# Kernel tuning notes

Measured on AMD Instinct MI355X. Metric: run time of the kernel, lower is better.

## Reference

```python
import jax, jax.numpy as jnp
import numpy as np

B, E, K, S, D, H, C = 8192, 8, 2, 32, 3072, 256, 100  # batch, experts, fix_points, img size, flat dim, hidden, classes


def setup_inputs() -> dict:
    key = jax.random.key(0)
    ks = jax.random.split(key, 6)
    return {
        "x": jax.random.normal(ks[0], (B, 3, S, S), jnp.float32),
        "coeffs_t": jax.random.uniform(ks[1], (K,), jnp.float32),
        "router_w": jax.random.normal(ks[2], (K, D, E), jnp.float32) * 0.02,
        "router_b": jnp.zeros((K, E), jnp.float32),
        "w1": jax.random.normal(ks[3], (E, K, D, H), jnp.float32) * 0.02,
        "b1": jnp.zeros((E, K, H), jnp.float32),
        "w2": jax.random.normal(ks[4], (E, K, H, C), jnp.float32) * 0.02,
        "b2": jnp.zeros((E, K, C), jnp.float32),
    }


def reference(x, coeffs_t, router_w, router_b, w1, b1, w2, b2):
    xf = x.reshape(x.shape[0], -1)  # [B, D]
    # Curve parameter blend: W = sum_k coeffs_t[k] * W_k (CurveParameter semantics)
    Wr = jnp.einsum('k,kde->de', coeffs_t, router_w)
    br = jnp.einsum('k,ke->e', coeffs_t, router_b)
    # Router: top-1 expert index per sample
    idx = jnp.argmax(xf @ Wr + br, axis=-1)  # [B] int
    # Blended expert weights
    W1 = jnp.einsum('k,ekdh->edh', coeffs_t, w1)
    B1 = jnp.einsum('k,ekh->eh', coeffs_t, b1)
    W2 = jnp.einsum('k,ekhc->ehc', coeffs_t, w2)
    B2 = jnp.einsum('k,ekc->ec', coeffs_t, b2)
    # Expert MLP (computed for all experts with static shapes, then top-1 gather;
    # identical math to torch's boolean-mask dispatch/scatter)
    h = jax.nn.gelu(jnp.einsum('bd,edh->beh', xf, W1) + B1, approximate=False)  # [B,E,H]
    o = jnp.einsum('beh,ehc->bec', h, W2) + B2  # [B,E,C]
    return jnp.take_along_axis(o, idx[:, None, None], axis=1)[:, 0, :]  # [B,C]
```

## Files before the change

### kernel.cpp

```cpp
#include <hip/hip_runtime.h>
#include <math.h>

#define B_  8192
#define E_  8
#define D_  3072
#define H_  256
#define C_  100
#define DH_ (D_*H_)
#define HC_ (H_*C_)
#define KS_ 4
#define KSEG_ (D_/KS_)
#define RKS_ 16
#define RSEG_ (D_/RKS_)
#define RB_ (B_/256)
#define NTMAX_ 136
#define NT2MAX_ 528
#define NCH_ (D_/32)
#define CHW_ 10240

#define MEGA_R_   (RB_*RKS_)
#define MEGA_W1_  (E_*NCH_)
#define MEGA_W2_  (C_*E_)
#define MEGA_BB_  3
#define MEGA_TOT_ (MEGA_R_ + MEGA_W1_ + MEGA_W2_ + MEGA_BB_)

typedef __attribute__((ext_vector_type(4))) float  f32x4;
typedef __attribute__((ext_vector_type(8))) __bf16 bf16x8;
typedef __attribute__((ext_vector_type(8))) unsigned short ush8;
typedef __attribute__((ext_vector_type(4))) unsigned short ush4;

#define GLOAD_LDS16(g, l) __builtin_amdgcn_global_load_lds( \
    (const __attribute__((address_space(1))) void*)(g),     \
    (__attribute__((address_space(3))) void*)(l), 16, 0, 0)

__device__ inline unsigned short bf16_rne(float f) {
    unsigned u = __builtin_bit_cast(unsigned, f);
    unsigned r = (u + 0x7FFFu + ((u >> 16) & 1u)) >> 16;
    return (unsigned short)r;
}
__device__ inline float bf16_f(unsigned short h) {
    unsigned u = ((unsigned)h) << 16;
    return __builtin_bit_cast(float, u);
}

#define MISC_B1_ (E_*H_/4)
#define MISC_B2_ (E_*C_/4)

__global__ __launch_bounds__(256) void mega_k(
        const float* __restrict__ x, const float* __restrict__ rw,
        const float* __restrict__ w1, const float* __restrict__ w2,
        const float* __restrict__ b1, const float* __restrict__ b2,
        unsigned short* __restrict__ Whi, unsigned short* __restrict__ Wlo,
        unsigned short* __restrict__ W2thi, unsigned short* __restrict__ W2tlo,
        float* __restrict__ B1b, float* __restrict__ B2b,
        double* __restrict__ lpart, const float* __restrict__ coeffs) {
    __shared__ char smem[36864];
    int bid = blockIdx.x;
    int t = threadIdx.x;

    if (bid < MEGA_R_) {
        float  (*xs)[64][33] = (float(*)[64][33])smem;
        double (*wls)[8]     = (double(*)[8])(smem + 33792);
        int w = t >> 6, lane = t & 63;
        int rowblk = (bid & (RB_ - 1)) * 256;
        int s2     = bid >> 5;
        int kbase  = s2 * RSEG_;
        int row0   = rowblk + w * 64;
        double c0 = (double)coeffs[0], c1 = (double)coeffs[1];

        double acc[8] = {0, 0, 0, 0, 0, 0, 0, 0};

        for (int kb = 0; kb < RSEG_; kb += 32) {
            #pragma unroll
            for (int it = 0; it < 8; it++) {
                int i = lane + it * 64;
                int r = i >> 3, c4 = i & 7;
                *(float4*)&xs[w][r][c4 * 4] =
                    *(const float4*)(x + (size_t)(row0 + r) * D_ + kbase + kb + c4 * 4);
            }
            if (w == 0) {
                #pragma unroll
                for (int it = 0; it < 4; it++) {
                    int i = lane + it * 64;
                    int k = i >> 3, ee = i & 7;
                    wls[k][ee] = c0 * (double)rw[(size_t)(kbase + kb + k) * 8 + ee]
                               + c1 * (double)rw[(size_t)(D_ + kbase + kb + k) * 8 + ee];
                }
            }
            __syncthreads();
            #pragma unroll
            for (int kk = 0; kk < 32; kk++) {
                double xv = (double)xs[w][lane][kk];
                double2 w01 = *(const double2*)&wls[kk][0];
                double2 w23 = *(const double2*)&wls[kk][2];
                double2 w45 = *(const double2*)&wls[kk][4];
                double2 w67 = *(const double2*)&wls[kk][6];
                acc[0] = fma(xv, w01.x, acc[0]);
                acc[1] = fma(xv, w01.y, acc[1]);
                acc[2] = fma(xv, w23.x, acc[2]);
                acc[3] = fma(xv, w23.y, acc[3]);
                acc[4] = fma(xv, w45.x, acc[4]);
                acc[5] = fma(xv, w45.y, acc[5]);
                acc[6] = fma(xv, w67.x, acc[6]);
                acc[7] = fma(xv, w67.y, acc[7]);
            }
            __syncthreads();
        }
        size_t base = ((size_t)s2 * B_ + row0 + lane) * 8;
        #pragma unroll
        for (int ee = 0; ee < 8; ee++) lpart[base + ee] = acc[ee];

    } else if (bid < MEGA_R_ + MEGA_W1_) {
        int lid = bid - MEGA_R_;
        int e  = lid / NCH_;
        int ci = lid - e * NCH_;
        int d0 = ci * 32;
        unsigned short* thi = (unsigned short*)smem;
        unsigned short* tlo = thi + 32 * 256;
        float c0 = coeffs[0], c1 = coeffs[1];
        const float* pa = w1 + ((size_t)(e * 2 + 0) * D_ + d0) * H_;
        const float* pb = w1 + ((size_t)(e * 2 + 1) * D_ + d0) * H_;
        #pragma unroll
        for (int it = 0; it < 8; it++) {
            int i4 = t + it * 256;
            float4 va = *(const float4*)(pa + (size_t)i4 * 4);
            float4 vb = *(const float4*)(pb + (size_t)i4 * 4);
            float vv[4] = {c0 * va.x + c1 * vb.x, c0 * va.y + c1 * vb.y,
                           c0 * va.z + c1 * vb.z, c0 * va.w + c1 * vb.w};
            unsigned short h4[4], l4[4];
            #pragma unroll
            for (int j = 0; j < 4; j++) {
                unsigned short hi = bf16_rne(vv[j]);
                h4[j] = hi;
                l4[j] = bf16_rne(vv[j] - bf16_f(hi));
            }
            *(ush4*)&thi[i4 * 4] = *(const ush4*)h4;
            *(ush4*)&tlo[i4 * 4] = *(const ush4*)l4;
        }
        __syncthreads();
        #pragma unroll
        for (int it = 0; it < 4; it++) {
            int j = t + it * 256;
            int h = j >> 2, d8 = (j & 3) * 8;
            unsigned short vh[8], vl[8];
            #pragma unroll
            for (int k2 = 0; k2 < 8; k2++) {
                vh[k2] = thi[(d8 + k2) * 256 + h];
                vl[k2] = tlo[(d8 + k2) * 256 + h];
            }
            size_t g = ((size_t)e * NCH_ + ci) * CHW_ + (size_t)h * 40 + d8;
            *(ush8*)(Whi + g) = *(const ush8*)vh;
            *(ush8*)(Wlo + g) = *(const ush8*)vl;
        }

    } else if (bid < MEGA_R_ + MEGA_W1_ + MEGA_W2_) {
        int lid = bid - (MEGA_R_ + MEGA_W1_);
        int c = lid % C_, e = lid / C_;
        int k = t;
        float c0 = coeffs[0], c1 = coeffs[1];
        float v = c0 * w2[((size_t)(e * 2 + 0) * H_ + k) * C_ + c]
                + c1 * w2[((size_t)(e * 2 + 1) * H_ + k) * C_ + c];
        unsigned short hi = bf16_rne(v);
        W2thi[(size_t)(e * C_ + c) * H_ + k] = hi;
        W2tlo[(size_t)(e * C_ + c) * H_ + k] = bf16_rne(v - bf16_f(hi));

    } else {
        int gid = (bid - (MEGA_R_ + MEGA_W1_ + MEGA_W2_)) * 256 + t;
        float c0 = coeffs[0], c1 = coeffs[1];
        if (gid < MISC_B1_) {
            const float4* p = (const float4*)b1;
            int e = gid / (H_ / 4), r = gid - e * (H_ / 4);
            float4 a = p[(e * 2 + 0) * (H_ / 4) + r];
            float4 bq = p[(e * 2 + 1) * (H_ / 4) + r];
            float4 o;
            o.x = c0 * a.x + c1 * bq.x;
            o.y = c0 * a.y + c1 * bq.y;
            o.z = c0 * a.z + c1 * bq.z;
            o.w = c0 * a.w + c1 * bq.w;
            ((float4*)B1b)[gid] = o;
        } else if (gid < MISC_B1_ + MISC_B2_) {
            int g2 = gid - MISC_B1_;
            const float4* p = (const float4*)b2;
            int e = g2 / (C_ / 4), r = g2 - e * (C_ / 4);
            float4 a = p[(e * 2 + 0) * (C_ / 4) + r];
            float4 bq = p[(e * 2 + 1) * (C_ / 4) + r];
            float4 o;
            o.x = c0 * a.x + c1 * bq.x;
            o.y = c0 * a.y + c1 * bq.y;
            o.z = c0 * a.z + c1 * bq.z;
            o.w = c0 * a.w + c1 * bq.w;
            ((float4*)B2b)[g2] = o;
        }
    }
}

__global__ __launch_bounds__(256) void argmax_hist_k(
        const double* __restrict__ lpart, const float* __restrict__ rb,
        const float* __restrict__ coeffs, int* __restrict__ idx,
        int* __restrict__ hist) {
    __shared__ int scnt[8];
    int t = threadIdx.x;
    if (t < 8) scnt[t] = 0;
    __syncthreads();
    int b = blockIdx.x * 256 + t;
    double c0 = (double)coeffs[0], c1 = (double)coeffs[1];
    double l[8];
    #pragma unroll
    for (int e = 0; e < 8; e++)
        l[e] = c0 * (double)rb[e] + c1 * (double)rb[8 + e];
    for (int s2 = 0; s2 < RKS_; s2++) {
        const double2* pp = (const double2*)(lpart + ((size_t)s2 * B_ + b) * 8);
        double2 v0 = pp[0], v1 = pp[1], v2 = pp[2], v3 = pp[3];
        l[0] += v0.x; l[1] += v0.y; l[2] += v1.x; l[3] += v1.y;
        l[4] += v2.x; l[5] += v2.y; l[6] += v3.x; l[7] += v3.y;
    }
    double best = -1e300;
    int bi = 0;
    #pragma unroll
    for (int e = 0; e < 8; e++)
        if (l[e] > best) { best = l[e]; bi = e; }
    idx[b] = bi;
    atomicAdd(&scnt[bi], 1);
    __syncthreads();
    if (t < 8) hist[blockIdx.x * 8 + t] = scnt[t];
}

__global__ __launch_bounds__(256) void scatter2_k(
        const int* __restrict__ idx, const int* __restrict__ hist,
        int* __restrict__ order, int* __restrict__ cnt, int* __restrict__ off,
        int* __restrict__ tmap, int* __restrict__ tmap2, int* __restrict__ ntl) {
    __shared__ int sbi[256];
    __shared__ int stot[8];
    __shared__ int sbase[8];
    int b0 = blockIdx.x, t = threadIdx.x;
    int b = b0 * 256 + t;
    int mybi = idx[b];
    sbi[t] = mybi;
    if (t < 8) {
        int tot = 0, pre = 0;
        for (int bb = 0; bb < RB_; bb++) {
            int h = hist[bb * 8 + t];
            if (bb < b0) pre += h;
            tot += h;
        }
        stot[t] = tot;
        sbase[t] = pre;
    }
    __syncthreads();
    if (t < 8) {
        int o = 0;
        for (int j = 0; j < t; j++) o += stot[j];
        sbase[t] += o;
    }
    __syncthreads();
    int rank = 0;
    for (int i = 0; i < 256; i++) {
        int v = sbi[i];
        rank += (i < t && v == mybi) ? 1 : 0;
    }
    order[sbase[mybi] + rank] = (mybi << 16) | b;

    if (b0 == 0 && t == 0) {
        int s = 0;
        for (int e = 0; e < E_; e++) { cnt[e] = stot[e]; off[e] = s; s += stot[e]; }
        int nt = 0;
        for (int e = 0; e < E_; e++)
            for (int t0 = 0; t0 < stot[e]; t0 += 64)
                tmap[nt++] = (e << 16) | t0;
        ntl[0] = nt;
        int nt2 = 0;
        for (int e = 0; e < E_; e++)
            for (int t0 = 0; t0 < stot[e]; t0 += 16)
                tmap2[nt2++] = (e << 16) | t0;
        ntl[1] = nt2;
    }
}

template<int MODE>
__global__ __launch_bounds__(256, 3) void gemm1_t(
        const float* __restrict__ x, const unsigned short* __restrict__ Whi,
        const unsigned short* __restrict__ Wlo, const int* __restrict__ order,
        const int* __restrict__ cnt, const int* __restrict__ off,
        const int* __restrict__ tmap, const int* __restrict__ ntl,
        float* __restrict__ dst) {
    int tid = blockIdx.y;
    if (tid >= ntl[0]) return;
    int tm = tmap[tid];
    int e = tm >> 16, tile0 = tm & 0xFFFF;
    int ce = cnt[e];
    int s = blockIdx.x;

    __shared__ int rows[64];
    __shared__ unsigned short xs_hi[64 * 40];
    __shared__ unsigned short xs_lo[64 * 40];
    __shared__ unsigned short ws_hi[256 * 40];
    __shared__ unsigned short ws_lo[256 * 40];

    int t = threadIdx.x;
    if (t < 64) {
        int i = tile0 + t;
        rows[t] = (i < ce) ? (order[off[e] + i] & 0xFFFF) : -1;
    }
    __syncthreads();
    int xrow0 = rows[0];

    int lane = t & 63, w = t >> 6;
    int lr = lane & 15, quad = lane >> 4;
    int kbase = s * KSEG_;
    int wuni = t & ~63;

    f32x4 acc[4][4];
    #pragma unroll
    for (int mt = 0; mt < 4; mt++)
        #pragma unroll
        for (int nt = 0; nt < 4; nt++)
            acc[mt][nt] = (f32x4){0.f, 0.f, 0.f, 0.f};

    for (int kb = 0; kb < KSEG_; kb += 32) {
        {
            int ci = (kbase + kb) >> 5;
            const unsigned short* ph = Whi + ((size_t)e * NCH_ + ci) * CHW_;
            const unsigned short* pl = Wlo + ((size_t)e * NCH_ + ci) * CHW_;
            #pragma unroll
            for (int j = 0; j < 5; j++) {
                GLOAD_LDS16(ph + ((size_t)(j * 256 + t)) * 8,
                            ws_hi + (size_t)(j * 256 + wuni) * 8);
                GLOAD_LDS16(pl + ((size_t)(j * 256 + t)) * 8,
                            ws_lo + (size_t)(j * 256 + wuni) * 8);
            }
        }
        #pragma unroll
        for (int it = 0; it < 2; it++) {
            int i = t + it * 256;
            int rr = i >> 3, sg = i & 7;
            int row = rows[rr];
            if (row < 0) row = xrow0;
            float4 v = *(const float4*)(x + (size_t)row * D_ + kbase + kb + sg * 4);
            unsigned short h4[4], l4[4];
            float vv[4] = {v.x, v.y, v.z, v.w};
            #pragma unroll
            for (int j = 0; j < 4; j++) {
                unsigned short hi = bf16_rne(vv[j]);
                h4[j] = hi;
                l4[j] = bf16_rne(vv[j] - bf16_f(hi));
            }
            *(ush4*)&xs_hi[rr * 40 + sg * 4] = *(const ush4*)h4;
            *(ush4*)&xs_lo[rr * 40 + sg * 4] = *(const ush4*)l4;
        }
        __syncthreads();

        bf16x8 ah[4], al[4], bh[4], bl[4];
        #pragma unroll
        for (int mt = 0; mt < 4; mt++) {
            ah[mt] = __builtin_bit_cast(bf16x8, *(const ush8*)&xs_hi[(mt * 16 + lr) * 40 + quad * 8]);
            al[mt] = __builtin_bit_cast(bf16x8, *(const ush8*)&xs_lo[(mt * 16 + lr) * 40 + quad * 8]);
        }
        #pragma unroll
        for (int nt = 0; nt < 4; nt++) {
            int col = w * 64 + nt * 16 + lr;
            bh[nt] = __builtin_bit_cast(bf16x8, *(const ush8*)&ws_hi[col * 40 + quad * 8]);
            bl[nt] = __builtin_bit_cast(bf16x8, *(const ush8*)&ws_lo[col * 40 + quad * 8]);
        }
        #pragma unroll
        for (int mt = 0; mt < 4; mt++)
            #pragma unroll
            for (int nt = 0; nt < 4; nt++) {
                acc[mt][nt] = __builtin_amdgcn_mfma_f32_16x16x32_bf16(ah[mt], bh[nt], acc[mt][nt], 0, 0, 0);
                acc[mt][nt] = __builtin_amdgcn_mfma_f32_16x16x32_bf16(al[mt], bh[nt], acc[mt][nt], 0, 0, 0);
                acc[mt][nt] = __builtin_amdgcn_mfma_f32_16x16x32_bf16(ah[mt], bl[nt], acc[mt][nt], 0, 0, 0);
                acc[mt][nt] = __builtin_amdgcn_mfma_f32_16x16x32_bf16(al[mt], bl[nt], acc[mt][nt], 0, 0, 0);
            }
        __syncthreads();
    }

    size_t p0 = (size_t)off[e] + tile0;
    if (MODE == 1) {
        float* dp = dst + ((size_t)s * B_ + p0) * H_;
        #pragma unroll
        for (int mt = 0; mt < 4; mt++) {
            int rl = mt * 16 + quad * 4;
            #pragma unroll
            for (int nt = 0; nt < 4; nt++) {
                int col = w * 64 + nt * 16 + lr;
                #pragma unroll
                for (int rg = 0; rg < 4; rg++) {
                    if (tile0 + rl + rg < ce)
                        dp[(size_t)(rl + rg) * H_ + col] = acc[mt][nt][rg];
                }
            }
        }
    } else {
        #pragma unroll
        for (int mt = 0; mt < 4; mt++) {
            int rl = mt * 16 + quad * 4;
            #pragma unroll
            for (int nt = 0; nt < 4; nt++) {
                int col = w * 64 + nt * 16 + lr;
                #pragma unroll
                for (int rg = 0; rg < 4; rg++) {
                    if (tile0 + rl + rg < ce)
                        atomicAdd(&dst[(p0 + rl + rg) * H_ + col], acc[mt][nt][rg]);
                }
            }
        }
    }
}

__global__ __launch_bounds__(256) void bias_gelu_k(
        float* __restrict__ hws, const float* __restrict__ B1b,
        const int* __restrict__ order) {
    int gid = blockIdx.x * 256 + threadIdx.x;
    int p = gid >> 6, c4 = (gid & 63) * 4;
    int e = order[p] >> 16;
    float4 v = *(const float4*)(hws + (size_t)p * H_ + c4);
    const float4 bb = *(const float4*)(B1b + e * H_ + c4);
    float pre[4] = {v.x + bb.x, v.y + bb.y, v.z + bb.z, v.w + bb.w};
    float4 o;
    o.x = 0.5f * pre[0] * (1.0f + erff(pre[0] * 0.70710678118654752440f));
    o.y = 0.5f * pre[1] * (1.0f + erff(pre[1] * 0.70710678118654752440f));
    o.z = 0.5f * pre[2] * (1.0f + erff(pre[2] * 0.70710678118654752440f));
    o.w = 0.5f * pre[3] * (1.0f + erff(pre[3] * 0.70710678118654752440f));
    *(float4*)(hws + (size_t)p * H_ + c4) = o;
}

template<int FUSE>
__global__ __launch_bounds__(256) void gemm2_t(
        const float* __restrict__ hsrc,
        const unsigned short* __restrict__ W2thi, const unsigned short* __restrict__ W2tlo,
        const float* __restrict__ B1b, const float* __restrict__ B2b,
        const int* __restrict__ order, const int* __restrict__ cnt,
        const int* __restrict__ off, const int* __restrict__ tmap2,
        const int* __restrict__ ntl, float* __restrict__ out) {
    int tid = blockIdx.x;
    if (tid >= ntl[1]) return;
    int tm = tmap2[tid];
    int e = tm >> 16, tile0 = tm & 0xFFFF;
    int ce = cnt[e];

    __shared__ int rows[16];
    __shared__ float red[3][64][28];

    int t = threadIdx.x;
    if (t < 16) {
        int i = tile0 + t;
        rows[t] = (i < ce) ? (order[off[e] + i] & 0xFFFF) : -1;
    }
    __syncthreads();

    int lane = t & 63, w = t >> 6;
    int m = lane & 15, q = lane >> 4;
    int p = off[e] + tile0 + ((tile0 + m < ce) ? m : 0);

    f32x4 acc[7];
    #pragma unroll
    for (int nt = 0; nt < 7; nt++) acc[nt] = (f32x4){0.f, 0.f, 0.f, 0.f};

    const unsigned short* w2h = W2thi + (size_t)e * C_ * H_;
    const unsigned short* w2l = W2tlo + (size_t)e * C_ * H_;

    #pragma unroll
    for (int si = 0; si < 2; si++) {
        int s = w * 2 + si;
        int k0 = s * 32 + q * 8;
        size_t o = (size_t)p * H_ + k0;
        float f[8];
        if (FUSE) {
            float4 a0 = *(const float4*)(hsrc + o);
            float4 a1 = *(const float4*)(hsrc + o + 4);
            #pragma unroll
            for (int s2 = 1; s2 < KS_; s2++) {
                const float* sp = hsrc + (size_t)s2 * B_ * H_ + o;
                float4 b0 = *(const float4*)sp;
                float4 b1v = *(const float4*)(sp + 4);
                a0.x += b0.x; a0.y += b0.y; a0.z += b0.z; a0.w += b0.w;
                a1.x += b1v.x; a1.y += b1v.y; a1.z += b1v.z; a1.w += b1v.w;
            }
            float4 bb0 = *(const float4*)(B1b + e * H_ + k0);
            float4 bb1 = *(const float4*)(B1b + e * H_ + k0 + 4);
            float pre[8] = {a0.x + bb0.x, a0.y + bb0.y, a0.z + bb0.z, a0.w + bb0.w,
                            a1.x + bb1.x, a1.y + bb1.y, a1.z + bb1.z, a1.w + bb1.w};
            #pragma unroll
            for (int j = 0; j < 8; j++)
                f[j] = 0.5f * pre[j] * (1.0f + erff(pre[j] * 0.70710678118654752440f));
        } else {
            float4 v0 = *(const float4*)(hsrc + o);
            float4 v1 = *(const float4*)(hsrc + o + 4);
            f[0] = v0.x; f[1] = v0.y; f[2] = v0.z; f[3] = v0.w;
            f[4] = v1.x; f[5] = v1.y; f[6] = v1.z; f[7] = v1.w;
        }
        unsigned short hh[8], lo[8];
        #pragma unroll
        for (int j = 0; j < 8; j++) {
            unsigned short hi = bf16_rne(f[j]);
            hh[j] = hi;
            lo[j] = bf16_rne(f[j] - bf16_f(hi));
        }
        bf16x8 ah = __builtin_bit_cast(bf16x8, *(const ush8*)hh);
        bf16x8 al = __builtin_bit_cast(bf16x8, *(const ush8*)lo);
        #pragma unroll
        for (int nt = 0; nt < 7; nt++) {
            size_t bo = (size_t)(nt * 16 + m) * H_ + k0;
            bf16x8 bh = __builtin_bit_cast(bf16x8, *(const ush8*)(w2h + bo));
            bf16x8 bl = __builtin_bit_cast(bf16x8, *(const ush8*)(w2l + bo));
            acc[nt] = __builtin_amdgcn_mfma_f32_16x16x32_bf16(ah, bh, acc[nt], 0, 0, 0);
            acc[nt] = __builtin_amdgcn_mfma_f32_16x16x32_bf16(al, bh, acc[nt], 0, 0, 0);
            acc[nt] = __builtin_amdgcn_mfma_f32_16x16x32_bf16(ah, bl, acc[nt], 0, 0, 0);
            acc[nt] = __builtin_amdgcn_mfma_f32_16x16x32_bf16(al, bl, acc[nt], 0, 0, 0);
        }
    }

    if (w > 0) {
        #pragma unroll
        for (int nt = 0; nt < 7; nt++)
            #pragma unroll
            for (int i = 0; i < 4; i++)
                red[w - 1][lane][nt * 4 + i] = acc[nt][i];
    }
    __syncthreads();
    if (w == 0) {
        #pragma unroll
        for (int nt = 0; nt < 7; nt++)
            #pragma unroll
            for (int i = 0; i < 4; i++)
                acc[nt][i] = ((acc[nt][i] + red[0][lane][nt * 4 + i])
                              + red[1][lane][nt * 4 + i]) + red[2][lane][nt * 4 + i];
        #pragma unroll
        for (int nt = 0; nt < 7; nt++) {
            int c = nt * 16 + m;
            if (c >= C_) continue;
            float bias = B2b[e * C_ + c];
            #pragma unroll
            for (int i = 0; i < 4; i++) {
                int grow = q * 4 + i;
                if (tile0 + grow < ce)
                    out[(size_t)rows[grow] * C_ + c] = acc[nt][i] + bias;
            }
        }
    }
}

extern "C" void kernel_launch(void* const* d_in, const int* in_sizes, int n_in,
                              void* d_out, int out_size, void* d_ws, size_t ws_size,
                              hipStream_t stream) {
    const float* x        = (const float*)d_in[0];
    const float* coeffs   = (const float*)d_in[1];
    const float* router_w = (const float*)d_in[2];
    const float* router_b = (const float*)d_in[3];
    const float* w1       = (const float*)d_in[4];
    const float* b1       = (const float*)d_in[5];
    const float* w2       = (const float*)d_in[6];
    const float* b2       = (const float*)d_in[7];
    float* out = (float*)d_out;

    unsigned short* Whi   = (unsigned short*)d_ws;
    unsigned short* Wlo   = Whi + (size_t)E_ * NCH_ * CHW_;
    unsigned short* W2thi = Wlo + (size_t)E_ * NCH_ * CHW_;
    unsigned short* W2tlo = W2thi + (size_t)E_ * C_ * H_;
    float* B1b  = (float*)(W2tlo + (size_t)E_ * C_ * H_);
    float* B2b  = B1b + (size_t)E_ * H_;
    int* order  = (int*)(B2b + E_ * C_);
    int* cnt    = order + B_;
    int* off    = cnt + E_;
    int* tmap   = off + E_;
    int* tmap2  = tmap + NTMAX_;
    int* ntl    = tmap2 + NT2MAX_;
    int* idx    = ntl + 4;
    int* hist   = idx + B_;
    float* hws  = (float*)(hist + 256);
    double* lpart = (double*)hws;

    size_t prefix_bytes = (size_t)((char*)hws - (char*)d_ws);
    int use_part = (ws_size >= prefix_bytes + (size_t)KS_ * B_ * H_ * sizeof(float) + 256) ? 1 : 0;

    mega_k<<<dim3(MEGA_TOT_), 256, 0, stream>>>(
        x, router_w, w1, w2, b1, b2, Whi, Wlo, W2thi, W2tlo, B1b, B2b,
        lpart, coeffs);

    argmax_hist_k<<<dim3(RB_), 256, 0, stream>>>(lpart, router_b, coeffs, idx, hist);
    scatter2_k<<<dim3(RB_), 256, 0, stream>>>(idx, hist, order, cnt, off,
                                              tmap, tmap2, ntl);

    if (use_part) {
        gemm1_t<1><<<dim3(KS_, NTMAX_), 256, 0, stream>>>(x, Whi, Wlo, order, cnt,
                                                          off, tmap, ntl, hws);
        gemm2_t<1><<<dim3(NT2MAX_), 256, 0, stream>>>(hws, W2thi, W2tlo, B1b, B2b,
                                                      order, cnt, off, tmap2, ntl, out);
    } else {
        hipMemsetAsync(hws, 0, (size_t)B_ * H_ * sizeof(float), stream);
        gemm1_t<0><<<dim3(KS_, NTMAX_), 256, 0, stream>>>(x, Whi, Wlo, order, cnt,
                                                          off, tmap, ntl, hws);
        bias_gelu_k<<<dim3(B_ * H_ / 4 / 256), 256, 0, stream>>>(hws, B1b, order);
        gemm2_t<0><<<dim3(NT2MAX_), 256, 0, stream>>>(hws, W2thi, W2tlo, B1b, B2b,
                                                      order, cnt, off, tmap2, ntl, out);
    }
}
```

Baseline: 323.0 us.

## Double-buffer router loads via async global-to-LDS with swizzle, shrink mega blocks

The router section of the preprocessing kernel now loads x tiles asynchronously into LDS with global_load_lds, double-buffered, and uses an XOR swizzle to avoid bank conflicts. The blended router weights for the next chunk are prefetched into registers and written to the other buffer after compute, which removes one barrier per iteration. Blocks shrink to 128 threads, with twice as many router blocks, and the other sections are adjusted to loop over twice as many elements. This aims to hide global load latency in the fp64 router GEMV, at the cost of more blocks and a more complex indexing scheme.

```diff
diff --git a/kernel.cpp b/kernel.cpp
--- a/kernel.cpp
+++ b/kernel.cpp
@@ -18,10 +18,10 @@
 #define NCH_ (D_/32)
 #define CHW_ 10240
 
-#define MEGA_R_   (RB_*RKS_)
+#define MEGA_R_   ((B_/128)*RKS_)
 #define MEGA_W1_  (E_*NCH_)
 #define MEGA_W2_  (C_*E_)
-#define MEGA_BB_  3
+#define MEGA_BB_  6
 #define MEGA_TOT_ (MEGA_R_ + MEGA_W1_ + MEGA_W2_ + MEGA_BB_)
 
 typedef __attribute__((ext_vector_type(4))) float  f32x4;
@@ -46,7 +46,7 @@
 #define MISC_B1_ (E_*H_/4)
 #define MISC_B2_ (E_*C_/4)
 
-__global__ __launch_bounds__(256) void mega_k(
+__global__ __launch_bounds__(128) void mega_k(
         const float* __restrict__ x, const float* __restrict__ rw,
         const float* __restrict__ w1, const float* __restrict__ w2,
         const float* __restrict__ b1, const float* __restrict__ b2,
@@ -59,42 +59,64 @@
     int t = threadIdx.x;
 
     if (bid < MEGA_R_) {
-        float  (*xs)[64][33] = (float(*)[64][33])smem;
-        double (*wls)[8]     = (double(*)[8])(smem + 33792);
+        float*  xs  = (float*)smem;
+        double* wls = (double*)(smem + 32768);
         int w = t >> 6, lane = t & 63;
-        int rowblk = (bid & (RB_ - 1)) * 256;
-        int s2     = bid >> 5;
+        int rowblk = (bid & 63) * 128;
+        int s2     = bid >> 6;
         int kbase  = s2 * RSEG_;
-        int row0   = rowblk + w * 64;
+        int row0w  = rowblk + w * 64;
         double c0 = (double)coeffs[0], c1 = (double)coeffs[1];
 
+        int c4L = (lane & 7) ^ ((lane >> 3) & 7);
+
         double acc[8] = {0, 0, 0, 0, 0, 0, 0, 0};
 
+        #pragma unroll
+        for (int j = 0; j < 8; j++) {
+            int r = j * 8 + (lane >> 3);
+            GLOAD_LDS16(x + (size_t)(row0w + r) * D_ + kbase + c4L * 4,
+                        smem + (size_t)w * 8192 + j * 1024);
+        }
+        {
+            #pragma unroll
+            for (int it = 0; it < 2; it++) {
+                int i = t + it * 128;
+                int k = i >> 3, ee = i & 7;
+                wls[k * 8 + ee] = c0 * (double)rw[(size_t)(kbase + k) * 8 + ee]
+                                + c1 * (double)rw[(size_t)(D_ + kbase + k) * 8 + ee];
+            }
+        }
+        __syncthreads();
+
+        int p = 0;
         for (int kb = 0; kb < RSEG_; kb += 32) {
-            #pragma unroll
-            for (int it = 0; it < 8; it++) {
-                int i = lane + it * 64;
-                int r = i >> 3, c4 = i & 7;
-                *(float4*)&xs[w][r][c4 * 4] =
-                    *(const float4*)(x + (size_t)(row0 + r) * D_ + kbase + kb + c4 * 4);
-            }
-            if (w == 0) {
+            int nxt = p ^ 1;
+            float rwa0 = 0.f, rwb0 = 0.f, rwa1 = 0.f, rwb1 = 0.f;
+            int more = (kb + 32 < RSEG_);
+            if (more) {
                 #pragma unroll
-                for (int it = 0; it < 4; it++) {
-                    int i = lane + it * 64;
-                    int k = i >> 3, ee = i & 7;
-                    wls[k][ee] = c0 * (double)rw[(size_t)(kbase + kb + k) * 8 + ee]
-                               + c1 * (double)rw[(size_t)(D_ + kbase + kb + k) * 8 + ee];
+                for (int j = 0; j < 8; j++) {
+                    int r = j * 8 + (lane >> 3);
+                    GLOAD_LDS16(x + (size_t)(row0w + r) * D_ + kbase + kb + 32 + c4L * 4,
+                                smem + (size_t)(nxt * 2 + w) * 8192 + j * 1024);
                 }
-            }
-            __syncthreads();
+                int i0 = t, i1 = t + 128;
+                rwa0 = rw[(size_t)(kbase + kb + 32 + (i0 >> 3)) * 8 + (i0 & 7)];
+                rwb0 = rw[(size_t)(D_ + kbase + kb + 32 + (i0 >> 3)) * 8 + (i0 & 7)];
+                rwa1 = rw[(size_t)(kbase + kb + 32 + (i1 >> 3)) * 8 + (i1 & 7)];
+                rwb1 = rw[(size_t)(D_ + kbase + kb + 32 + (i1 >> 3)) * 8 + (i1 & 7)];
+            }
+
+            const float*  xw = xs + (size_t)(p * 2 + w) * 2048 + lane * 32;
+            const double* wp = wls + (size_t)p * 256;
             #pragma unroll
             for (int kk = 0; kk < 32; kk++) {
-                double xv = (double)xs[w][lane][kk];
-                double2 w01 = *(const double2*)&wls[kk][0];
-                double2 w23 = *(const double2*)&wls[kk][2];
-                double2 w45 = *(const double2*)&wls[kk][4];
-                double2 w67 = *(const double2*)&wls[kk][6];
+                double xv = (double)xw[((((kk >> 2) ^ (lane & 7)) << 2) + (kk & 3))];
+                double2 w01 = *(const double2*)&wp[kk * 8 + 0];
+                double2 w23 = *(const double2*)&wp[kk * 8 + 2];
+                double2 w45 = *(const double2*)&wp[kk * 8 + 4];
+                double2 w67 = *(const double2*)&wp[kk * 8 + 6];
                 acc[0] = fma(xv, w01.x, acc[0]);
                 acc[1] = fma(xv, w01.y, acc[1]);
                 acc[2] = fma(xv, w23.x, acc[2]);
@@ -104,9 +126,17 @@
                 acc[6] = fma(xv, w67.x, acc[6]);
                 acc[7] = fma(xv, w67.y, acc[7]);
             }
+
+            if (more) {
+                double* wn = wls + (size_t)nxt * 256;
+                int i0 = t, i1 = t + 128;
+                wn[(i0 >> 3) * 8 + (i0 & 7)] = c0 * (double)rwa0 + c1 * (double)rwb0;
+                wn[(i1 >> 3) * 8 + (i1 & 7)] = c0 * (double)rwa1 + c1 * (double)rwb1;
+            }
             __syncthreads();
-        }
-        size_t base = ((size_t)s2 * B_ + row0 + lane) * 8;
+            p = nxt;
+        }
+        size_t base = ((size_t)s2 * B_ + row0w + lane) * 8;
         #pragma unroll
         for (int ee = 0; ee < 8; ee++) lpart[base + ee] = acc[ee];
 
@@ -121,8 +151,8 @@
         const float* pa = w1 + ((size_t)(e * 2 + 0) * D_ + d0) * H_;
         const float* pb = w1 + ((size_t)(e * 2 + 1) * D_ + d0) * H_;
         #pragma unroll
-        for (int it = 0; it < 8; it++) {
-            int i4 = t + it * 256;
+        for (int it = 0; it < 16; it++) {
+            int i4 = t + it * 128;
             float4 va = *(const float4*)(pa + (size_t)i4 * 4);
             float4 vb = *(const float4*)(pb + (size_t)i4 * 4);
             float vv[4] = {c0 * va.x + c1 * vb.x, c0 * va.y + c1 * vb.y,
@@ -139,8 +169,8 @@
         }
         __syncthreads();
         #pragma unroll
-        for (int it = 0; it < 4; it++) {
-            int j = t + it * 256;
+        for (int it = 0; it < 8; it++) {
+            int j = t + it * 128;
             int h = j >> 2, d8 = (j & 3) * 8;
             unsigned short vh[8], vl[8];
             #pragma unroll
@@ -156,16 +186,19 @@
     } else if (bid < MEGA_R_ + MEGA_W1_ + MEGA_W2_) {
         int lid = bid - (MEGA_R_ + MEGA_W1_);
         int c = lid % C_, e = lid / C_;
-        int k = t;
         float c0 = coeffs[0], c1 = coeffs[1];
-        float v = c0 * w2[((size_t)(e * 2 + 0) * H_ + k) * C_ + c]
-                + c1 * w2[((size_t)(e * 2 + 1) * H_ + k) * C_ + c];
-        unsigned short hi = bf16_rne(v);
-        W2thi[(size_t)(e * C_ + c) * H_ + k] = hi;
-        W2tlo[(size_t)(e * C_ + c) * H_ + k] = bf16_rne(v - bf16_f(hi));
+        #pragma unroll
+        for (int kk2 = 0; kk2 < 2; kk2++) {
+            int k = t + kk2 * 128;
+            float v = c0 * w2[((size_t)(e * 2 + 0) * H_ + k) * C_ + c]
+                    + c1 * w2[((size_t)(e * 2 + 1) * H_ + k) * C_ + c];
+            unsigned short hi = bf16_rne(v);
+            W2thi[(size_t)(e * C_ + c) * H_ + k] = hi;
+            W2tlo[(size_t)(e * C_ + c) * H_ + k] = bf16_rne(v - bf16_f(hi));
+        }
 
     } else {
-        int gid = (bid - (MEGA_R_ + MEGA_W1_ + MEGA_W2_)) * 256 + t;
+        int gid = (bid - (MEGA_R_ + MEGA_W1_ + MEGA_W2_)) * 128 + t;
         float c0 = coeffs[0], c1 = coeffs[1];
         if (gid < MISC_B1_) {
             const float4* p = (const float4*)b1;
@@ -572,7 +605,7 @@
     size_t prefix_bytes = (size_t)((char*)hws - (char*)d_ws);
     int use_part = (ws_size >= prefix_bytes + (size_t)KS_ * B_ * H_ * sizeof(float) + 256) ? 1 : 0;
 
-    mega_k<<<dim3(MEGA_TOT_), 256, 0, stream>>>(
+    mega_k<<<dim3(MEGA_TOT_), 128, 0, stream>>>(
         x, router_w, w1, w2, b1, b2, Whi, Wlo, W2thi, W2tlo, B1b, B2b,
         lpart, coeffs);
 
```

After: 462.6 us. 1.43x slower.
